# Kernel tuning notes

Measured on AMD Instinct MI355X. Metric: run time of the kernel, lower is better.

The kernel has to match this reference:

```python
import jax, jax.numpy as jnp
import numpy as np

V = 100000
E = 1600000
BN_EPS = 1e-5


def spmm(edge_index, vals, X):
    # X: (V, Cin, B); sparse L @ X via scatter-add. y[r] += w * X[c]
    rows, cols = edge_index[0], edge_index[1]
    return jnp.zeros_like(X).at[rows].add(vals[:, None, None] * X[cols])


def cheb_conv(x, edge_index, vals, w, b=None):
    # x: (B, Cin, V), w: (K, Cin, Cout) -> (B, Cout, V)
    K = w.shape[0]
    x0 = jnp.transpose(x, (2, 1, 0))  # (V, Cin, B)
    xs = [x0]
    if K > 1:
        x1 = spmm(edge_index, vals, x0)
        xs.append(x1)
        for _ in range(2, K):
            x2 = 2.0 * spmm(edge_index, vals, x1) - x0
            xs.append(x2)
            x0, x1 = x1, x2
    xk = jnp.stack(xs)  # (K, V, Cin, B)
    out = jnp.einsum('kvcb,kco->bov', xk, w)
    if b is not None:
        out = out + b[None, :, None]
    return out


def batch_norm(x, g, b):
    # training-mode BatchNorm1d on (B, C, V): stats over (B, V), biased var
    m = jnp.mean(x, axis=(0, 2), keepdims=True)
    v = jnp.var(x, axis=(0, 2), keepdims=True)
    return g[None, :, None] * (x - m) * jax.lax.rsqrt(v + BN_EPS) + b[None, :, None]


def setup_inputs() -> dict:
    key = jax.random.key(0)
    ks = jax.random.split(key, 8)
    x = jax.random.normal(ks[0], (4, 32, V), dtype=jnp.float32)
    edge_index = jax.random.randint(ks[1], (2, E), 0, V, dtype=jnp.int32)
    # small values keep the K=4 Chebyshev recursion well-scaled
    lap_vals = 0.1 * jax.random.normal(ks[2], (E,), dtype=jnp.float32)
    def w(k, K, cin, cout):
        s = 1.0 / np.sqrt(K * cin)
        return s * jax.random.normal(k, (K, cin, cout), dtype=jnp.float32)
    return {
        'x': x, 'edge_index': edge_index, 'lap_vals': lap_vals,
        'in_bn_g': jnp.ones((32,), jnp.float32), 'in_bn_b': jnp.zeros((32,), jnp.float32),
        'in_w': w(ks[3], 4, 32, 64), 'in_b': jnp.zeros((64,), jnp.float32),
        'h0_bn_g': jnp.ones((64,), jnp.float32), 'h0_bn_b': jnp.zeros((64,), jnp.float32),
        'h0_w': w(ks[4], 4, 64, 64), 'h0_b': jnp.zeros((64,), jnp.float32),
        'h1_bn_g': jnp.ones((64,), jnp.float32), 'h1_bn_b': jnp.zeros((64,), jnp.float32),
        'h1_w': w(ks[5], 4, 64, 32), 'h1_b': jnp.zeros((32,), jnp.float32),
    }


def reference(x, edge_index, lap_vals, in_bn_g, in_bn_b, in_w, in_b,
              h0_bn_g, h0_bn_b, h0_w, h0_b, h1_bn_g, h1_bn_b, h1_w, h1_b):
    xn = batch_norm(x, in_bn_g, in_bn_b)
    out = cheb_conv(xn, edge_index, lap_vals, in_w, in_b)
    # hidden layer 0
    out = jax.nn.relu(out)
    out = batch_norm(out, h0_bn_g, h0_bn_b)
    out = cheb_conv(out, edge_index, lap_vals, h0_w, h0_b)
    # hidden layer 1
    out = jax.nn.relu(out)
    out = batch_norm(out, h1_bn_g, h1_bn_b)
    out = cheb_conv(out, edge_index, lap_vals, h1_w, h1_b)
    # in_channels == out_channels -> Identity shortcut on the BN'ed input
    return jax.nn.relu(out + xn)
```

## Files before the change

kernel.cpp:

```cpp
#include <hip/hip_runtime.h>
#include <cstdint>
#include <cstddef>

#define VN 100000
#define EN 1600000
static constexpr float BN_EPS_F = 1e-5f;
static constexpr float INV_N = 1.0f / 400000.0f;

using short8 = __attribute__((ext_vector_type(8))) short;
using f32x4  = __attribute__((ext_vector_type(4))) float;

__device__ __forceinline__ float bf_lo(unsigned int p) {
  return __builtin_bit_cast(float, p << 16);
}
__device__ __forceinline__ float bf_hi(unsigned int p) {
  return __builtin_bit_cast(float, p & 0xffff0000u);
}
__device__ __forceinline__ float bf1(unsigned short u) {
  return __builtin_bit_cast(float, ((unsigned int)u) << 16);
}
__device__ __forceinline__ unsigned short f2bf(float f) {
  unsigned int x = __builtin_bit_cast(unsigned int, f);
  x += 0x7fffu + ((x >> 16) & 1u);
  return (unsigned short)(x >> 16);
}
__device__ __forceinline__ unsigned int pack2(float a, float b) {
  return (unsigned int)f2bf(a) | ((unsigned int)f2bf(b) << 16);
}

template <int EPL>
__device__ __forceinline__ void gather_accum(int start, int end,
    const int* __restrict__ cs, const float* __restrict__ vs,
    const unsigned short* __restrict__ X, int XS, int lane, float* acc) {
  int e = start;
  for (; e + 4 <= end; e += 4) {
    const int c0 = cs[e], c1 = cs[e + 1], c2 = cs[e + 2], c3 = cs[e + 3];
    const float w0 = vs[e], w1 = vs[e + 1], w2 = vs[e + 2], w3 = vs[e + 3];
    if constexpr (EPL == 4) {
      const uint2 q0 = *reinterpret_cast<const uint2*>(X + (size_t)c0 * XS + lane * 4);
      const uint2 q1 = *reinterpret_cast<const uint2*>(X + (size_t)c1 * XS + lane * 4);
      const uint2 q2 = *reinterpret_cast<const uint2*>(X + (size_t)c2 * XS + lane * 4);
      const uint2 q3 = *reinterpret_cast<const uint2*>(X + (size_t)c3 * XS + lane * 4);
      acc[0] += w0 * bf_lo(q0.x) + w1 * bf_lo(q1.x) + w2 * bf_lo(q2.x) + w3 * bf_lo(q3.x);
      acc[1] += w0 * bf_hi(q0.x) + w1 * bf_hi(q1.x) + w2 * bf_hi(q2.x) + w3 * bf_hi(q3.x);
      acc[2] += w0 * bf_lo(q0.y) + w1 * bf_lo(q1.y) + w2 * bf_lo(q2.y) + w3 * bf_lo(q3.y);
      acc[3] += w0 * bf_hi(q0.y) + w1 * bf_hi(q1.y) + w2 * bf_hi(q2.y) + w3 * bf_hi(q3.y);
    } else {
      const unsigned int q0 = *reinterpret_cast<const unsigned int*>(X + (size_t)c0 * XS + lane * 2);
      const unsigned int q1 = *reinterpret_cast<const unsigned int*>(X + (size_t)c1 * XS + lane * 2);
      const unsigned int q2 = *reinterpret_cast<const unsigned int*>(X + (size_t)c2 * XS + lane * 2);
      const unsigned int q3 = *reinterpret_cast<const unsigned int*>(X + (size_t)c3 * XS + lane * 2);
      acc[0] += w0 * bf_lo(q0) + w1 * bf_lo(q1) + w2 * bf_lo(q2) + w3 * bf_lo(q3);
      acc[1] += w0 * bf_hi(q0) + w1 * bf_hi(q1) + w2 * bf_hi(q2) + w3 * bf_hi(q3);
    }
  }
  for (; e < end; e++) {
    const int c0 = cs[e];
    const float w0 = vs[e];
    if constexpr (EPL == 4) {
      const uint2 q0 = *reinterpret_cast<const uint2*>(X + (size_t)c0 * XS + lane * 4);
      acc[0] += w0 * bf_lo(q0.x);
      acc[1] += w0 * bf_hi(q0.x);
      acc[2] += w0 * bf_lo(q0.y);
      acc[3] += w0 * bf_hi(q0.y);
    } else {
      const unsigned int q0 = *reinterpret_cast<const unsigned int*>(X + (size_t)c0 * XS + lane * 2);
      acc[0] += w0 * bf_lo(q0);
      acc[1] += w0 * bf_hi(q0);
    }
  }
}

__global__ __launch_bounds__(256) void stats_x_kernel(const float* __restrict__ x,
                                                      float* __restrict__ stats) {
  const int p = blockIdx.x & 127;
  const int chunk = blockIdx.x >> 7;
  const int c = p & 31, b = p >> 5;
  const float* base = x + ((size_t)b * 32 + c) * VN + chunk * 12500;
  float s = 0.f, s2 = 0.f;
  for (int i = threadIdx.x; i < 12500; i += 256) {
    float v = base[i];
    s += v; s2 += v * v;
  }
  __shared__ float r1[256], r2[256];
  r1[threadIdx.x] = s; r2[threadIdx.x] = s2;
  __syncthreads();
  for (int off = 128; off > 0; off >>= 1) {
    if (threadIdx.x < off) {
      r1[threadIdx.x] += r1[threadIdx.x + off];
      r2[threadIdx.x] += r2[threadIdx.x + off];
    }
    __syncthreads();
  }
  if (threadIdx.x == 0) {
    atomicAdd(&stats[c], r1[0]);
    atomicAdd(&stats[64 + c], r2[0]);
  }
}

__global__ void finalize_stats_kernel(float* __restrict__ stats,
                                      const float* __restrict__ g,
                                      const float* __restrict__ beta, int C) {
  int c = threadIdx.x;
  if (c < C) {
    float m = stats[c] * INV_N;
    float var = stats[64 + c] * INV_N - m * m;
    float sc = g[c] * rsqrtf(var + BN_EPS_F);
    stats[128 + c] = sc;
    stats[192 + c] = beta[c] - m * sc;
  }
}

__global__ __launch_bounds__(128) void bn_transpose_kernel(const float* __restrict__ x,
                                                           const float* __restrict__ stats,
                                                           unsigned short* __restrict__ xn) {
  const int tid = threadIdx.x;
  const int b = tid >> 5, c = tid & 31;
  const int v0 = blockIdx.x * 64;
  const float sc = stats[128 + c], sh = stats[192 + c];
  const float* src = x + ((size_t)b * 32 + c) * VN;
  for (int i = 0; i < 64; i++) {
    int v = v0 + i;
    if (v < VN) xn[(size_t)v * 128 + tid] = f2bf(sc * src[v] + sh);
  }
}

__global__ __launch_bounds__(256) void pack_wb_kernel(const float* __restrict__ W,
                                                      unsigned short* __restrict__ Wb,
                                                      int Cin, int Cout) {
  const int i = blockIdx.x * 256 + threadIdx.x;
  const int KC = Cin >> 5, T = Cout >> 4;
  const int tot = 4 * KC * T * 512;
  if (i >= tot) return;
  const int j = i & 7;
  const int l = (i >> 3) & 63;
  const int rem = i >> 9;
  const int t = rem % T;
  const int kc = (rem / T) % KC;
  const int k = rem / (T * KC);
  const int c = kc * 32 + (l >> 4) * 8 + j;
  const int o = t * 16 + (l & 15);
  Wb[i] = f2bf(W[((size_t)k * Cin + c) * Cout + o]);
}

__global__ __launch_bounds__(256) void hist_kernel(const int* __restrict__ rows,
                                                   int* __restrict__ cnt) {
  int i = blockIdx.x * blockDim.x + threadIdx.x;
  const int stride = gridDim.x * blockDim.x;
  for (; i < EN; i += stride) atomicAdd(&cnt[rows[i]], 1);
}

__global__ __launch_bounds__(256) void scan1_kernel(const int* __restrict__ cnt,
                                                    int* __restrict__ rp,
                                                    int* __restrict__ chunkSums) {
  __shared__ int sh[256];
  const int t = threadIdx.x;
  const int base = blockIdx.x * 2048 + t * 8;
  int vals[8]; int tot = 0;
#pragma unroll
  for (int i = 0; i < 8; i++) {
    int idx = base + i;
    int v = (idx < VN) ? cnt[idx] : 0;
    vals[i] = v; tot += v;
  }
  sh[t] = tot;
  __syncthreads();
  for (int off = 1; off < 256; off <<= 1) {
    int v = (t >= off) ? sh[t - off] : 0;
    __syncthreads();
    sh[t] += v;
    __syncthreads();
  }
  int run = sh[t] - tot;
#pragma unroll
  for (int i = 0; i < 8; i++) {
    int idx = base + i;
    if (idx < VN) rp[idx] = run;
    run += vals[i];
  }
  if (t == 255) chunkSums[blockIdx.x] = sh[255];
}

__global__ void scan2_kernel(const int* __restrict__ chunkSums,
                             int* __restrict__ chunkOff,
                             int* __restrict__ rp, int nChunks) {
  if (threadIdx.x == 0 && blockIdx.x == 0) {
    int off = 0;
    for (int j = 0; j < nChunks; j++) { chunkOff[j] = off; off += chunkSums[j]; }
    rp[VN] = off;
  }
}

__global__ __launch_bounds__(256) void scan3_kernel(int* __restrict__ rp,
                                                    const int* __restrict__ chunkOff,
                                                    int* __restrict__ fill) {
  int i = blockIdx.x * 256 + threadIdx.x;
  if (i < VN) {
    int v = rp[i] + chunkOff[i >> 11];
    rp[i] = v;
    fill[i] = v;
  }
}

__global__ __launch_bounds__(256) void fill_kernel(const int* __restrict__ rows,
                                                   const int* __restrict__ cols,
                                                   const float* __restrict__ lap,
                                                   int* __restrict__ fill,
                                                   int* __restrict__ cols_s,
                                                   float* __restrict__ vals_s) {
  int i = blockIdx.x * blockDim.x + threadIdx.x;
  const int stride = gridDim.x * blockDim.x;
  for (; i < EN; i += stride) {
    int r = rows[i];
    int pos = atomicAdd(&fill[r], 1);
    cols_s[pos] = cols[i];
    vals_s[pos] = lap[i];
  }
}

__global__ __launch_bounds__(256) void row_sum_kernel(const int* __restrict__ rp,
                                                      const float* __restrict__ vs,
                                                      float* __restrict__ rowsum) {
  const int i = blockIdx.x * 256 + threadIdx.x;
  if (i >= VN) return;
  const int s = rp[i], e = rp[i + 1];
  float acc = 0.f;
  for (int j = s; j < e; j++) acc += vs[j];
  rowsum[i] = acc;
}

template <int EPL, int MODE, bool AFFE, bool AFFP>
__global__ __launch_bounds__(256, 8) void spmm_kernel(const int* __restrict__ rp,
                                                   const int* __restrict__ cs,
                                                   const float* __restrict__ vs,
                                                   const unsigned short* __restrict__ X, int XS,
                                                   const unsigned short* __restrict__ P, int PS,
                                                   const unsigned short* __restrict__ Q, int QS,
                                                   unsigned short* __restrict__ Y, int YS,
                                                   const float* __restrict__ bnp,
                                                   const float* __restrict__ rowsum) {
  const int lane = threadIdx.x & 63;
  const int row = blockIdx.x * 4 + (threadIdx.x >> 6);
  const int start = rp[row], end = rp[row + 1];
  float acc[EPL];
#pragma unroll
  for (int j = 0; j < EPL; j++) acc[j] = 0.f;
  gather_accum<EPL>(start, end, cs, vs, X, XS, lane, acc);

  if constexpr (EPL == 4) {
    float4 sc, sh;
    if constexpr (AFFE || AFFP) {
      const int c0 = (lane * 4) & 63;
      sc = *reinterpret_cast<const float4*>(bnp + c0);
      sh = *reinterpret_cast<const float4*>(bnp + 64 + c0);
    }
    float r0 = acc[0], r1 = acc[1], r2 = acc[2], r3 = acc[3];
    if constexpr (AFFE) {
      const float rs = rowsum[row];
      r0 = sc.x * r0 + rs * sh.x;
      r1 = sc.y * r1 + rs * sh.y;
      r2 = sc.z * r2 + rs * sh.z;
      r3 = sc.w * r3 + rs * sh.w;
    }
    if constexpr (MODE == 1) {
      const uint2 p = *reinterpret_cast<const uint2*>(P + (size_t)row * PS + lane * 4);
      float p0 = bf_lo(p.x), p1 = bf_hi(p.x), p2 = bf_lo(p.y), p3 = bf_hi(p.y);
      if constexpr (AFFP) {
        p0 = p0 * sc.x + sh.x;
        p1 = p1 * sc.y + sh.y;
        p2 = p2 * sc.z + sh.z;
        p3 = p3 * sc.w + sh.w;
      }
      r0 = 2.f * r0 - p0;
      r1 = 2.f * r1 - p1;
      r2 = 2.f * r2 - p2;
      r3 = 2.f * r3 - p3;
    }
    uint2 r;
    r.x = pack2(r0, r1);
    r.y = pack2(r2, r3);
    *reinterpret_cast<uint2*>(Y + (size_t)row * YS + lane * 4) = r;
  } else {
    float r0 = acc[0], r1 = acc[1];
    if constexpr (MODE == 1) {
      const unsigned int p = *reinterpret_cast<const unsigned int*>(P + (size_t)row * PS + lane * 2);
      r0 = 2.f * r0 - bf_lo(p);
      r1 = 2.f * r1 - bf_hi(p);
    } else if constexpr (MODE == 2) {
      const unsigned int p = *reinterpret_cast<const unsigned int*>(P + (size_t)row * PS + lane * 2);
      r0 = 2.f * r0 + bf_lo(p);
      r1 = 2.f * r1 + bf_hi(p);
    } else if constexpr (MODE == 3) {
      const unsigned int p = *reinterpret_cast<const unsigned int*>(P + (size_t)row * PS + lane * 2);
      const unsigned int qq = *reinterpret_cast<const unsigned int*>(Q + (size_t)row * QS + lane * 2);
      r0 = 2.f * r0 - bf_lo(qq) + bf_lo(p);
      r1 = 2.f * r1 - bf_hi(qq) + bf_hi(p);
    } else if constexpr (MODE == 4) {
      const unsigned int p = *reinterpret_cast<const unsigned int*>(P + (size_t)row * PS + lane * 2);
      const unsigned int qq = *reinterpret_cast<const unsigned int*>(Q + (size_t)row * QS + lane * 2);
      r0 = r0 - bf_lo(qq) + bf_lo(p);
      r1 = r1 - bf_hi(qq) + bf_hi(p);
    }
    *reinterpret_cast<unsigned int*>(Y + (size_t)row * YS + lane * 2) = pack2(r0, r1);
  }
}

template <int Cin, int Cout, int X0S, int X1S, int X2S, bool AFF0>
__global__ __launch_bounds__(256, 8) void fused_cheb_kernel(const int* __restrict__ rp,
                                                         const int* __restrict__ cs,
                                                         const float* __restrict__ vs,
                                                         const unsigned short* __restrict__ X0,
                                                         const unsigned short* __restrict__ X1,
                                                         const unsigned short* __restrict__ X2,
                                                         unsigned short* __restrict__ OUT,
                                                         const unsigned short* __restrict__ Wb,
                                                         const float* __restrict__ Bias,
                                                         const float* __restrict__ bnp) {
  constexpr int EPL = Cin * 4 / 64;
  constexpr int ROWSH = Cin * 4;
  __shared__ unsigned short t3s[4 * ROWSH];
  const int lane = threadIdx.x & 63;
  const int wv = threadIdx.x >> 6;
  const int row0 = blockIdx.x * 4;
  const int row = row0 + wv;

  float g[EPL];
#pragma unroll
  for (int j = 0; j < EPL; j++) g[j] = 0.f;
  const int start = rp[row], end = rp[row + 1];
  gather_accum<EPL>(start, end, cs, vs, X2, X2S, lane, g);
  {
    unsigned int* tw = reinterpret_cast<unsigned int*>(t3s + wv * ROWSH);
    if constexpr (EPL == 4) {
      const uint2 p = *reinterpret_cast<const uint2*>(X1 + (size_t)row * X1S + lane * 4);
      tw[lane * 2]     = pack2(2.f * g[0] - bf_lo(p.x), 2.f * g[1] - bf_hi(p.x));
      tw[lane * 2 + 1] = pack2(2.f * g[2] - bf_lo(p.y), 2.f * g[3] - bf_hi(p.y));
    } else {
      const unsigned int p = *reinterpret_cast<const unsigned int*>(X1 + (size_t)row * X1S + lane * 2);
      tw[lane] = pack2(2.f * g[0] - bf_lo(p), 2.f * g[1] - bf_hi(p));
    }
  }
  __syncthreads();

  constexpr int KC = Cin / 32;
  constexpr int T = Cout / 16;
  const int col = lane & 15, quad = lane >> 4;
  const int t = wv % T;
  const int ar = col >> 2, ab = col & 3;

  const unsigned short* xa0 = X0 + (size_t)(row0 + ar) * X0S + ab * Cin + quad * 8;
  const unsigned short* xa1 = X1 + (size_t)(row0 + ar) * X1S + ab * Cin + quad * 8;
  const unsigned short* xa2 = X2 + (size_t)(row0 + ar) * X2S + ab * Cin + quad * 8;
  const unsigned short* wb = Wb + (size_t)t * 512 + lane * 8;

  f32x4 acc = {0.f, 0.f, 0.f, 0.f};
#pragma unroll
  for (int kc = 0; kc < KC; kc++) {
    short8 af;
    if constexpr (AFF0) {
      const short8 raw = *reinterpret_cast<const short8*>(xa0 + kc * 32);
      const int cb = quad * 8 + kc * 32;
      const float4 s0 = *reinterpret_cast<const float4*>(bnp + cb);
      const float4 s1 = *reinterpret_cast<const float4*>(bnp + cb + 4);
      const float4 t0 = *reinterpret_cast<const float4*>(bnp + 64 + cb);
      const float4 t1 = *reinterpret_cast<const float4*>(bnp + 64 + cb + 4);
      const float scv[8] = {s0.x, s0.y, s0.z, s0.w, s1.x, s1.y, s1.z, s1.w};
      const float shv[8] = {t0.x, t0.y, t0.z, t0.w, t1.x, t1.y, t1.z, t1.w};
#pragma unroll
      for (int j = 0; j < 8; j++) {
        float v = bf1((unsigned short)raw[j]) * scv[j] + shv[j];
        af[j] = (short)f2bf(v);
      }
    } else {
      af = *reinterpret_cast<const short8*>(xa0 + kc * 32);
    }
    const short8 bf = *reinterpret_cast<const short8*>(wb + (size_t)(0 * KC + kc) * T * 512);
    acc = __builtin_amdgcn_mfma_f32_16x16x32_bf16(af, bf, acc, 0, 0, 0);
  }
#pragma unroll
  for (int kc = 0; kc < KC; kc++) {
    const short8 af = *reinterpret_cast<const short8*>(xa1 + kc * 32);
    const short8 bf = *reinterpret_cast<const short8*>(wb + (size_t)(1 * KC + kc) * T * 512);
    acc = __builtin_amdgcn_mfma_f32_16x16x32_bf16(af, bf, acc, 0, 0, 0);
  }
#pragma unroll
  for (int kc = 0; kc < KC; kc++) {
    const short8 af = *reinterpret_cast<const short8*>(xa2 + kc * 32);
    const short8 bf = *reinterpret_cast<const short8*>(wb + (size_t)(2 * KC + kc) * T * 512);
    acc = __builtin_amdgcn_mfma_f32_16x16x32_bf16(af, bf, acc, 0, 0, 0);
  }
#pragma unroll
  for (int kc = 0; kc < KC; kc++) {
    const short8 af = *reinterpret_cast<const short8*>(&t3s[ar * ROWSH + ab * Cin + kc * 32 + quad * 8]);
    const short8 bf = *reinterpret_cast<const short8*>(wb + (size_t)(3 * KC + kc) * T * 512);
    acc = __builtin_amdgcn_mfma_f32_16x16x32_bf16(af, bf, acc, 0, 0, 0);
  }
  __syncthreads();

  if (T == 4 || wv < 2) {
    const int og = t * 16 + col;
    const float bs = Bias[og];
#pragma unroll
    for (int r = 0; r < 4; r++) {
      const float val = fmaxf(acc[r] + bs, 0.f);
      OUT[(size_t)(row0 + quad) * 256 + r * Cout + og] = f2bf(val);
    }
  }
}

__global__ __launch_bounds__(256, 8) void gemm_z_kernel(const unsigned short* __restrict__ A,
                                                        const unsigned short* __restrict__ Wb,
                                                        const float* __restrict__ Bias,
                                                        unsigned short* __restrict__ zA,
                                                        unsigned short* __restrict__ zB,
                                                        const float* __restrict__ bnp) {
  const int lane = threadIdx.x & 63;
  const int wv = threadIdx.x >> 6;
  const int row0 = blockIdx.x * 4;
  const int col = lane & 15, quad = lane >> 4;
  const int ar = col >> 2, ab = col & 3;
  const unsigned short* xa = A + (size_t)(row0 + ar) * 256 + ab * 64 + quad * 8;
  const unsigned short* wb = Wb + (size_t)wv * 4 * 512 + lane * 8;
  unsigned short* zr = (wv < 2) ? (zA + (size_t)wv * VN * 128)
                                : (zB + (size_t)(wv - 2) * VN * 128);
  short8 afr[2];
#pragma unroll
  for (int kc = 0; kc < 2; kc++) {
    const short8 raw = *reinterpret_cast<const short8*>(xa + kc * 32);
    const int cb = quad * 8 + kc * 32;
    const float4 s0 = *reinterpret_cast<const float4*>(bnp + cb);
    const float4 s1 = *reinterpret_cast<const float4*>(bnp + cb + 4);
    const float4 t0 = *reinterpret_cast<const float4*>(bnp + 64 + cb);
    const float4 t1 = *reinterpret_cast<const float4*>(bnp + 64 + cb + 4);
    const float scv[8] = {s0.x, s0.y, s0.z, s0.w, s1.x, s1.y, s1.z, s1.w};
    const float shv[8] = {t0.x, t0.y, t0.z, t0.w, t1.x, t1.y, t1.z, t1.w};
#pragma unroll
    for (int j = 0; j < 8; j++) {
      float v = bf1((unsigned short)raw[j]) * scv[j] + shv[j];
      afr[kc][j] = (short)f2bf(v);
    }
  }
#pragma unroll
  for (int t = 0; t < 2; t++) {
    f32x4 acc = {0.f, 0.f, 0.f, 0.f};
#pragma unroll
    for (int kc = 0; kc < 2; kc++) {
      const short8 bf = *reinterpret_cast<const short8*>(wb + (size_t)(kc * 2 + t) * 512);
      acc = __builtin_amdgcn_mfma_f32_16x16x32_bf16(afr[kc], bf, acc, 0, 0, 0);
    }
    const int og = t * 16 + col;
    const float bs = (wv == 0) ? Bias[og] : 0.f;
#pragma unroll
    for (int r = 0; r < 4; r++) {
      zr[(size_t)(row0 + quad) * 128 + r * 32 + og] = f2bf(acc[r] + bs);
    }
  }
}

__global__ __launch_bounds__(256) void stats_out_kernel(const unsigned short* __restrict__ SRC,
                                                        float* __restrict__ stats) {
  const int tid = threadIdx.x;
  const int per = (VN + gridDim.x - 1) / gridDim.x;
  const int v0 = blockIdx.x * per;
  const int v1 = (v0 + per < VN) ? (v0 + per) : VN;
  float s = 0.f, s2 = 0.f;
  for (int v = v0; v < v1; v++) {
    float val = bf1(SRC[(size_t)v * 256 + tid]);
    s += val; s2 += val * val;
  }
  __shared__ float r1[256], r2[256];
  r1[tid] = s; r2[tid] = s2;
  __syncthreads();
  if (tid < 64) {
    float a = r1[tid] + r1[tid + 64] + r1[tid + 128] + r1[tid + 192];
    float b = r2[tid] + r2[tid + 64] + r2[tid + 128] + r2[tid + 192];
    atomicAdd(&stats[tid], a);
    atomicAdd(&stats[64 + tid], b);
  }
}

__global__ __launch_bounds__(256) void final_kernel(const unsigned short* __restrict__ SRC,
                                                    const unsigned short* __restrict__ xn,
                                                    float* __restrict__ out) {
  const int lane = threadIdx.x & 63;
  const int grp = threadIdx.x >> 6;
  const int v = blockIdx.x * 64 + lane;
  if (v >= VN) return;
  for (int ob = grp; ob < 128; ob += 4) {
    float val = bf1(SRC[(size_t)v * 128 + ob]) + bf1(xn[(size_t)v * 128 + ob]);
    val = fmaxf(val, 0.f);
    out[(size_t)ob * VN + v] = val;
  }
}

static constexpr size_t align_up(size_t x) { return (x + 255) & ~(size_t)255; }
static constexpr size_t OFF_RP    = 0;
static constexpr size_t OFF_FILL  = align_up(OFF_RP + (size_t)(VN + 1) * 4);
static constexpr size_t OFF_CHS   = align_up(OFF_FILL + (size_t)VN * 4);
static constexpr size_t OFF_CHO   = align_up(OFF_CHS + 256);
static constexpr size_t OFF_STATS = align_up(OFF_CHO + 256);
static constexpr size_t OFF_WP    = align_up(OFF_STATS + 1024);
static constexpr size_t OFF_CS    = align_up(OFF_WP + 32768 * 2);
static constexpr size_t OFF_VS    = align_up(OFF_CS + (size_t)EN * 4);
static constexpr size_t OFF_XN    = align_up(OFF_VS + (size_t)EN * 4);
static constexpr size_t OFF_XL    = align_up(OFF_XN + (size_t)VN * 128 * 2);
static constexpr size_t OFF_A     = align_up(OFF_XL + (size_t)VN * 256 * 2);
static constexpr size_t OFF_B     = align_up(OFF_A + (size_t)VN * 256 * 2);
static constexpr size_t OFF_END   = OFF_B + (size_t)VN * 256 * 2;

extern "C" void kernel_launch(void* const* d_in, const int* in_sizes, int n_in,
                              void* d_out, int out_size, void* d_ws, size_t ws_size,
                              hipStream_t stream) {
  if (ws_size < OFF_END) return;

  const float* x       = (const float*)d_in[0];
  const int*   rows    = (const int*)d_in[1];
  const int*   cols    = rows + EN;
  const float* lap     = (const float*)d_in[2];
  const float* in_bn_g = (const float*)d_in[3];
  const float* in_bn_b = (const float*)d_in[4];
  const float* in_w    = (const float*)d_in[5];
  const float* in_b    = (const float*)d_in[6];
  const float* h0_bn_g = (const float*)d_in[7];
  const float* h0_bn_b = (const float*)d_in[8];
  const float* h0_w    = (const float*)d_in[9];
  const float* h0_b    = (const float*)d_in[10];
  const float* h1_bn_g = (const float*)d_in[11];
  const float* h1_bn_b = (const float*)d_in[12];
  const float* h1_w    = (const float*)d_in[13];
  const float* h1_b    = (const float*)d_in[14];
  float* outp = (float*)d_out;

  char* ws = (char*)d_ws;
  int*   rp     = (int*)(ws + OFF_RP);
  int*   fill   = (int*)(ws + OFF_FILL);
  float* rowsum = (float*)(ws + OFF_FILL);
  int*   chS    = (int*)(ws + OFF_CHS);
  int*   chO    = (int*)(ws + OFF_CHO);
  float* stats  = (float*)(ws + OFF_STATS);
  unsigned short* wbIn = (unsigned short*)(ws + OFF_WP);
  unsigned short* wbH0 = wbIn + 8192;
  unsigned short* wbH1 = wbH0 + 16384;
  int*   cs     = (int*)(ws + OFF_CS);
  float* vs     = (float*)(ws + OFF_VS);
  unsigned short* xn = (unsigned short*)(ws + OFF_XN);
  unsigned short* XL = (unsigned short*)(ws + OFF_XL);
  unsigned short* A  = (unsigned short*)(ws + OFF_A);
  unsigned short* B  = (unsigned short*)(ws + OFF_B);
  const float* bnp = stats + 128;

  const int nChunks = (VN + 2047) / 2048;

  pack_wb_kernel<<<32, 256, 0, stream>>>(in_w, wbIn, 32, 64);
  pack_wb_kernel<<<64, 256, 0, stream>>>(h0_w, wbH0, 64, 64);
  pack_wb_kernel<<<32, 256, 0, stream>>>(h1_w, wbH1, 64, 32);

  hipMemsetAsync(stats, 0, 1024, stream);
  stats_x_kernel<<<1024, 256, 0, stream>>>(x, stats);
  finalize_stats_kernel<<<1, 64, 0, stream>>>(stats, in_bn_g, in_bn_b, 32);
  bn_transpose_kernel<<<1563, 128, 0, stream>>>(x, stats, xn);

  hipMemsetAsync(fill, 0, (size_t)VN * 4, stream);
  hist_kernel<<<2048, 256, 0, stream>>>(rows, fill);
  scan1_kernel<<<nChunks, 256, 0, stream>>>(fill, rp, chS);
  scan2_kernel<<<1, 64, 0, stream>>>(chS, chO, rp, nChunks);
  scan3_kernel<<<(VN + 255) / 256, 256, 0, stream>>>(rp, chO, fill);
  fill_kernel<<<2048, 256, 0, stream>>>(rows, cols, lap, fill, cs, vs);
  row_sum_kernel<<<(VN + 255) / 256, 256, 0, stream>>>(rp, vs, rowsum);

  unsigned short* XLa = XL;
  unsigned short* XLb = XL + (size_t)VN * 128;
  spmm_kernel<2, 0, false, false><<<VN / 4, 256, 0, stream>>>(
      rp, cs, vs, xn, 128, nullptr, 0, nullptr, 0, XLa, 128, nullptr, nullptr);
  spmm_kernel<2, 1, false, false><<<VN / 4, 256, 0, stream>>>(
      rp, cs, vs, XLa, 128, xn, 128, nullptr, 0, XLb, 128, nullptr, nullptr);
  fused_cheb_kernel<32, 64, 128, 128, 128, false><<<VN / 4, 256, 0, stream>>>(
      rp, cs, vs, xn, XLa, XLb, A, wbIn, in_b, nullptr);
  hipMemsetAsync(stats, 0, 1024, stream);
  stats_out_kernel<<<256, 256, 0, stream>>>(A, stats);
  finalize_stats_kernel<<<1, 64, 0, stream>>>(stats, h0_bn_g, h0_bn_b, 64);

  spmm_kernel<4, 0, true, false><<<VN / 4, 256, 0, stream>>>(
      rp, cs, vs, A, 256, nullptr, 0, nullptr, 0, XL, 256, bnp, rowsum);
  spmm_kernel<4, 1, false, true><<<VN / 4, 256, 0, stream>>>(
      rp, cs, vs, XL, 256, A, 256, nullptr, 0, B, 256, bnp, nullptr);
  fused_cheb_kernel<64, 64, 256, 256, 256, true><<<VN / 4, 256, 0, stream>>>(
      rp, cs, vs, A, XL, B, A, wbH0, h0_b, bnp);
  hipMemsetAsync(stats, 0, 1024, stream);
  stats_out_kernel<<<256, 256, 0, stream>>>(A, stats);
  finalize_stats_kernel<<<1, 64, 0, stream>>>(stats, h1_bn_g, h1_bn_b, 64);

  {
    unsigned short* z0 = XL;
    unsigned short* z1 = XL + (size_t)VN * 128;
    unsigned short* z2 = B;
    unsigned short* z3 = B + (size_t)VN * 128;
    gemm_z_kernel<<<VN / 4, 256, 0, stream>>>(A, wbH1, h1_b, z0, z2, bnp);
    spmm_kernel<2, 2, false, false><<<VN / 4, 256, 0, stream>>>(
        rp, cs, vs, z3, 128, z2, 128, nullptr, 0, z2, 128, nullptr, nullptr);
    spmm_kernel<2, 3, false, false><<<VN / 4, 256, 0, stream>>>(
        rp, cs, vs, z2, 128, z1, 128, z3, 128, z1, 128, nullptr, nullptr);
    spmm_kernel<2, 4, false, false><<<VN / 4, 256, 0, stream>>>(
        rp, cs, vs, z1, 128, z0, 128, z2, 128, z0, 128, nullptr, nullptr);
    final_kernel<<<1563, 256, 0, stream>>>(z0, xn, outp);
  }
}
```

Before: 1.665 ms.

## Fold batch-norm affine into packed weights and biases; unroll gather by eight

Moves the per-element batch-norm scale and shift out of the fused Chebyshev and gemm_z kernels. The scale is folded into the packed bf16 weights, and the shift times the weights is folded into per-k bias vectors computed by a small new kernel. Weight packing for the hidden layers now runs after their stats are finalized. Separately, the sparse gather loop is unrolled to eight edges so more loads are in flight. The change drops per-element conversion work but alters bf16 rounding order and adds two tiny serial launches per layer.

```diff
diff --git a/kernel.cpp b/kernel.cpp
--- a/kernel.cpp
+++ b/kernel.cpp
@@ -33,40 +33,77 @@
     const int* __restrict__ cs, const float* __restrict__ vs,
     const unsigned short* __restrict__ X, int XS, int lane, float* acc) {
   int e = start;
-  for (; e + 4 <= end; e += 4) {
-    const int c0 = cs[e], c1 = cs[e + 1], c2 = cs[e + 2], c3 = cs[e + 3];
-    const float w0 = vs[e], w1 = vs[e + 1], w2 = vs[e + 2], w3 = vs[e + 3];
-    if constexpr (EPL == 4) {
-      const uint2 q0 = *reinterpret_cast<const uint2*>(X + (size_t)c0 * XS + lane * 4);
-      const uint2 q1 = *reinterpret_cast<const uint2*>(X + (size_t)c1 * XS + lane * 4);
-      const uint2 q2 = *reinterpret_cast<const uint2*>(X + (size_t)c2 * XS + lane * 4);
-      const uint2 q3 = *reinterpret_cast<const uint2*>(X + (size_t)c3 * XS + lane * 4);
-      acc[0] += w0 * bf_lo(q0.x) + w1 * bf_lo(q1.x) + w2 * bf_lo(q2.x) + w3 * bf_lo(q3.x);
-      acc[1] += w0 * bf_hi(q0.x) + w1 * bf_hi(q1.x) + w2 * bf_hi(q2.x) + w3 * bf_hi(q3.x);
-      acc[2] += w0 * bf_lo(q0.y) + w1 * bf_lo(q1.y) + w2 * bf_lo(q2.y) + w3 * bf_lo(q3.y);
-      acc[3] += w0 * bf_hi(q0.y) + w1 * bf_hi(q1.y) + w2 * bf_hi(q2.y) + w3 * bf_hi(q3.y);
-    } else {
-      const unsigned int q0 = *reinterpret_cast<const unsigned int*>(X + (size_t)c0 * XS + lane * 2);
-      const unsigned int q1 = *reinterpret_cast<const unsigned int*>(X + (size_t)c1 * XS + lane * 2);
-      const unsigned int q2 = *reinterpret_cast<const unsigned int*>(X + (size_t)c2 * XS + lane * 2);
-      const unsigned int q3 = *reinterpret_cast<const unsigned int*>(X + (size_t)c3 * XS + lane * 2);
-      acc[0] += w0 * bf_lo(q0) + w1 * bf_lo(q1) + w2 * bf_lo(q2) + w3 * bf_lo(q3);
-      acc[1] += w0 * bf_hi(q0) + w1 * bf_hi(q1) + w2 * bf_hi(q2) + w3 * bf_hi(q3);
-    }
-  }
-  for (; e < end; e++) {
-    const int c0 = cs[e];
-    const float w0 = vs[e];
-    if constexpr (EPL == 4) {
-      const uint2 q0 = *reinterpret_cast<const uint2*>(X + (size_t)c0 * XS + lane * 4);
-      acc[0] += w0 * bf_lo(q0.x);
-      acc[1] += w0 * bf_hi(q0.x);
-      acc[2] += w0 * bf_lo(q0.y);
-      acc[3] += w0 * bf_hi(q0.y);
-    } else {
-      const unsigned int q0 = *reinterpret_cast<const unsigned int*>(X + (size_t)c0 * XS + lane * 2);
-      acc[0] += w0 * bf_lo(q0);
-      acc[1] += w0 * bf_hi(q0);
+  if constexpr (EPL == 4) {
+    for (; e + 8 <= end; e += 8) {
+      uint2 q[8]; float w[8];
+#pragma unroll
+      for (int u = 0; u < 8; u++) {
+        q[u] = *reinterpret_cast<const uint2*>(X + (size_t)cs[e + u] * XS + lane * 4);
+        w[u] = vs[e + u];
+      }
+#pragma unroll
+      for (int u = 0; u < 8; u++) {
+        acc[0] += w[u] * bf_lo(q[u].x);
+        acc[1] += w[u] * bf_hi(q[u].x);
+        acc[2] += w[u] * bf_lo(q[u].y);
+        acc[3] += w[u] * bf_hi(q[u].y);
+      }
+    }
+    for (; e + 4 <= end; e += 4) {
+      uint2 q[4]; float w[4];
+#pragma unroll
+      for (int u = 0; u < 4; u++) {
+        q[u] = *reinterpret_cast<const uint2*>(X + (size_t)cs[e + u] * XS + lane * 4);
+        w[u] = vs[e + u];
+      }
+#pragma unroll
+      for (int u = 0; u < 4; u++) {
+        acc[0] += w[u] * bf_lo(q[u].x);
+        acc[1] += w[u] * bf_hi(q[u].x);
+        acc[2] += w[u] * bf_lo(q[u].y);
+        acc[3] += w[u] * bf_hi(q[u].y);
+      }
+    }
+    for (; e < end; e++) {
+      const uint2 q = *reinterpret_cast<const uint2*>(X + (size_t)cs[e] * XS + lane * 4);
+      const float w = vs[e];
+      acc[0] += w * bf_lo(q.x);
+      acc[1] += w * bf_hi(q.x);
+      acc[2] += w * bf_lo(q.y);
+      acc[3] += w * bf_hi(q.y);
+    }
+  } else {
+    for (; e + 8 <= end; e += 8) {
+      unsigned int q[8]; float w[8];
+#pragma unroll
+      for (int u = 0; u < 8; u++) {
+        q[u] = *reinterpret_cast<const unsigned int*>(X + (size_t)cs[e + u] * XS + lane * 2);
+        w[u] = vs[e + u];
+      }
+#pragma unroll
+      for (int u = 0; u < 8; u++) {
+        acc[0] += w[u] * bf_lo(q[u]);
+        acc[1] += w[u] * bf_hi(q[u]);
+      }
+    }
+    for (; e + 4 <= end; e += 4) {
+      unsigned int q[4]; float w[4];
+#pragma unroll
+      for (int u = 0; u < 4; u++) {
+        q[u] = *reinterpret_cast<const unsigned int*>(X + (size_t)cs[e + u] * XS + lane * 2);
+        w[u] = vs[e + u];
+      }
+#pragma unroll
+      for (int u = 0; u < 4; u++) {
+        acc[0] += w[u] * bf_lo(q[u]);
+        acc[1] += w[u] * bf_hi(q[u]);
+      }
+    }
+    for (; e < end; e++) {
+      const unsigned int q = *reinterpret_cast<const unsigned int*>(X + (size_t)cs[e] * XS + lane * 2);
+      const float w = vs[e];
+      acc[0] += w * bf_lo(q);
+      acc[1] += w * bf_hi(q);
     }
   }
 }
@@ -127,7 +164,9 @@
 
 __global__ __launch_bounds__(256) void pack_wb_kernel(const float* __restrict__ W,
                                                       unsigned short* __restrict__ Wb,
-                                                      int Cin, int Cout) {
+                                                      int Cin, int Cout,
+                                                      const float* __restrict__ scale,
+                                                      int kmask) {
   const int i = blockIdx.x * 256 + threadIdx.x;
   const int KC = Cin >> 5, T = Cout >> 4;
   const int tot = 4 * KC * T * 512;
@@ -140,7 +179,23 @@
   const int k = rem / (T * KC);
   const int c = kc * 32 + (l >> 4) * 8 + j;
   const int o = t * 16 + (l & 15);
-  Wb[i] = f2bf(W[((size_t)k * Cin + c) * Cout + o]);
+  float w = W[((size_t)k * Cin + c) * Cout + o];
+  if (scale != nullptr && ((kmask >> k) & 1)) w *= scale[c];
+  Wb[i] = f2bf(w);
+}
+
+__global__ void bias_fold_kernel(const float* __restrict__ W,
+                                 const float* __restrict__ b0,
+                                 const float* __restrict__ stats,
+                                 float* __restrict__ out,
+                                 int Cin, int Cout, int K) {
+  const int i = threadIdx.x;
+  if (i >= K * Cout) return;
+  const int k = i / Cout, o = i % Cout;
+  const float* sh = stats + 192;
+  float acc = (k == 0) ? b0[o] : 0.f;
+  for (int c = 0; c < Cin; c++) acc += sh[c] * W[((size_t)k * Cin + c) * Cout + o];
+  out[i] = acc;
 }
 
 __global__ __launch_bounds__(256) void hist_kernel(const int* __restrict__ rows,
@@ -305,7 +360,7 @@
   }
 }
 
-template <int Cin, int Cout, int X0S, int X1S, int X2S, bool AFF0>
+template <int Cin, int Cout, int X0S, int X1S, int X2S>
 __global__ __launch_bounds__(256, 8) void fused_cheb_kernel(const int* __restrict__ rp,
                                                          const int* __restrict__ cs,
                                                          const float* __restrict__ vs,
@@ -314,8 +369,7 @@
                                                          const unsigned short* __restrict__ X2,
                                                          unsigned short* __restrict__ OUT,
                                                          const unsigned short* __restrict__ Wb,
-                                                         const float* __restrict__ Bias,
-                                                         const float* __restrict__ bnp) {
+                                                         const float* __restrict__ Bias) {
   constexpr int EPL = Cin * 4 / 64;
   constexpr int ROWSH = Cin * 4;
   __shared__ unsigned short t3s[4 * ROWSH];
@@ -356,24 +410,7 @@
   f32x4 acc = {0.f, 0.f, 0.f, 0.f};
 #pragma unroll
   for (int kc = 0; kc < KC; kc++) {
-    short8 af;
-    if constexpr (AFF0) {
-      const short8 raw = *reinterpret_cast<const short8*>(xa0 + kc * 32);
-      const int cb = quad * 8 + kc * 32;
-      const float4 s0 = *reinterpret_cast<const float4*>(bnp + cb);
-      const float4 s1 = *reinterpret_cast<const float4*>(bnp + cb + 4);
-      const float4 t0 = *reinterpret_cast<const float4*>(bnp + 64 + cb);
-      const float4 t1 = *reinterpret_cast<const float4*>(bnp + 64 + cb + 4);
-      const float scv[8] = {s0.x, s0.y, s0.z, s0.w, s1.x, s1.y, s1.z, s1.w};
-      const float shv[8] = {t0.x, t0.y, t0.z, t0.w, t1.x, t1.y, t1.z, t1.w};
-#pragma unroll
-      for (int j = 0; j < 8; j++) {
-        float v = bf1((unsigned short)raw[j]) * scv[j] + shv[j];
-        af[j] = (short)f2bf(v);
-      }
-    } else {
-      af = *reinterpret_cast<const short8*>(xa0 + kc * 32);
-    }
+    const short8 af = *reinterpret_cast<const short8*>(xa0 + kc * 32);
     const short8 bf = *reinterpret_cast<const short8*>(wb + (size_t)(0 * KC + kc) * T * 512);
     acc = __builtin_amdgcn_mfma_f32_16x16x32_bf16(af, bf, acc, 0, 0, 0);
   }
@@ -410,10 +447,9 @@
 
 __global__ __launch_bounds__(256, 8) void gemm_z_kernel(const unsigned short* __restrict__ A,
                                                         const unsigned short* __restrict__ Wb,
-                                                        const float* __restrict__ Bias,
+                                                        const float* __restrict__ zb,
                                                         unsigned short* __restrict__ zA,
-                                                        unsigned short* __restrict__ zB,
-                                                        const float* __restrict__ bnp) {
+                                                        unsigned short* __restrict__ zB) {
   const int lane = threadIdx.x & 63;
   const int wv = threadIdx.x >> 6;
   const int row0 = blockIdx.x * 4;
@@ -423,33 +459,17 @@
   const unsigned short* wb = Wb + (size_t)wv * 4 * 512 + lane * 8;
   unsigned short* zr = (wv < 2) ? (zA + (size_t)wv * VN * 128)
                                 : (zB + (size_t)(wv - 2) * VN * 128);
-  short8 afr[2];
-#pragma unroll
-  for (int kc = 0; kc < 2; kc++) {
-    const short8 raw = *reinterpret_cast<const short8*>(xa + kc * 32);
-    const int cb = quad * 8 + kc * 32;
-    const float4 s0 = *reinterpret_cast<const float4*>(bnp + cb);
-    const float4 s1 = *reinterpret_cast<const float4*>(bnp + cb + 4);
-    const float4 t0 = *reinterpret_cast<const float4*>(bnp + 64 + cb);
-    const float4 t1 = *reinterpret_cast<const float4*>(bnp + 64 + cb + 4);
-    const float scv[8] = {s0.x, s0.y, s0.z, s0.w, s1.x, s1.y, s1.z, s1.w};
-    const float shv[8] = {t0.x, t0.y, t0.z, t0.w, t1.x, t1.y, t1.z, t1.w};
-#pragma unroll
-    for (int j = 0; j < 8; j++) {
-      float v = bf1((unsigned short)raw[j]) * scv[j] + shv[j];
-      afr[kc][j] = (short)f2bf(v);
-    }
-  }
+  const short8 af0 = *reinterpret_cast<const short8*>(xa);
+  const short8 af1 = *reinterpret_cast<const short8*>(xa + 32);
 #pragma unroll
   for (int t = 0; t < 2; t++) {
     f32x4 acc = {0.f, 0.f, 0.f, 0.f};
-#pragma unroll
-    for (int kc = 0; kc < 2; kc++) {
-      const short8 bf = *reinterpret_cast<const short8*>(wb + (size_t)(kc * 2 + t) * 512);
-      acc = __builtin_amdgcn_mfma_f32_16x16x32_bf16(afr[kc], bf, acc, 0, 0, 0);
-    }
+    const short8 bf0 = *reinterpret_cast<const short8*>(wb + (size_t)(0 * 2 + t) * 512);
+    const short8 bf1 = *reinterpret_cast<const short8*>(wb + (size_t)(1 * 2 + t) * 512);
+    acc = __builtin_amdgcn_mfma_f32_16x16x32_bf16(af0, bf0, acc, 0, 0, 0);
+    acc = __builtin_amdgcn_mfma_f32_16x16x32_bf16(af1, bf1, acc, 0, 0, 0);
     const int og = t * 16 + col;
-    const float bs = (wv == 0) ? Bias[og] : 0.f;
+    const float bs = zb[wv * 32 + og];
 #pragma unroll
     for (int r = 0; r < 4; r++) {
       zr[(size_t)(row0 + quad) * 128 + r * 32 + og] = f2bf(acc[r] + bs);
@@ -499,7 +519,8 @@
 static constexpr size_t OFF_CHS   = align_up(OFF_FILL + (size_t)VN * 4);
 static constexpr size_t OFF_CHO   = align_up(OFF_CHS + 256);
 static constexpr size_t OFF_STATS = align_up(OFF_CHO + 256);
-static constexpr size_t OFF_WP    = align_up(OFF_STATS + 1024);
+static constexpr size_t OFF_BIAS  = align_up(OFF_STATS + 1024);
+static constexpr size_t OFF_WP    = align_up(OFF_BIAS + 1024);
 static constexpr size_t OFF_CS    = align_up(OFF_WP + 32768 * 2);
 static constexpr size_t OFF_VS    = align_up(OFF_CS + (size_t)EN * 4);
 static constexpr size_t OFF_XN    = align_up(OFF_VS + (size_t)EN * 4);
@@ -538,6 +559,7 @@
   int*   chS    = (int*)(ws + OFF_CHS);
   int*   chO    = (int*)(ws + OFF_CHO);
   float* stats  = (float*)(ws + OFF_STATS);
+  float* biasF  = (float*)(ws + OFF_BIAS);
   unsigned short* wbIn = (unsigned short*)(ws + OFF_WP);
   unsigned short* wbH0 = wbIn + 8192;
   unsigned short* wbH1 = wbH0 + 16384;
@@ -551,9 +573,7 @@
 
   const int nChunks = (VN + 2047) / 2048;
 
-  pack_wb_kernel<<<32, 256, 0, stream>>>(in_w, wbIn, 32, 64);
-  pack_wb_kernel<<<64, 256, 0, stream>>>(h0_w, wbH0, 64, 64);
-  pack_wb_kernel<<<32, 256, 0, stream>>>(h1_w, wbH1, 64, 32);
+  pack_wb_kernel<<<32, 256, 0, stream>>>(in_w, wbIn, 32, 64, nullptr, 0);
 
   hipMemsetAsync(stats, 0, 1024, stream);
   stats_x_kernel<<<1024, 256, 0, stream>>>(x, stats);
@@ -574,28 +594,34 @@
       rp, cs, vs, xn, 128, nullptr, 0, nullptr, 0, XLa, 128, nullptr, nullptr);
   spmm_kernel<2, 1, false, false><<<VN / 4, 256, 0, stream>>>(
       rp, cs, vs, XLa, 128, xn, 128, nullptr, 0, XLb, 128, nullptr, nullptr);
-  fused_cheb_kernel<32, 64, 128, 128, 128, false><<<VN / 4, 256, 0, stream>>>(
-      rp, cs, vs, xn, XLa, XLb, A, wbIn, in_b, nullptr);
+  fused_cheb_kernel<32, 64, 128, 128, 128><<<VN / 4, 256, 0, stream>>>(
+      rp, cs, vs, xn, XLa, XLb, A, wbIn, in_b);
   hipMemsetAsync(stats, 0, 1024, stream);
   stats_out_kernel<<<256, 256, 0, stream>>>(A, stats);
   finalize_stats_kernel<<<1, 64, 0, stream>>>(stats, h0_bn_g, h0_bn_b, 64);
+
+  pack_wb_kernel<<<64, 256, 0, stream>>>(h0_w, wbH0, 64, 64, bnp, 0x1);
+  bias_fold_kernel<<<1, 128, 0, stream>>>(h0_w, h0_b, stats, biasF, 64, 64, 1);
 
   spmm_kernel<4, 0, true, false><<<VN / 4, 256, 0, stream>>>(
       rp, cs, vs, A, 256, nullptr, 0, nullptr, 0, XL, 256, bnp, rowsum);
   spmm_kernel<4, 1, false, true><<<VN / 4, 256, 0, stream>>>(
       rp, cs, vs, XL, 256, A, 256, nullptr, 0, B, 256, bnp, nullptr);
-  fused_cheb_kernel<64, 64, 256, 256, 256, true><<<VN / 4, 256, 0, stream>>>(
-      rp, cs, vs, A, XL, B, A, wbH0, h0_b, bnp);
+  fused_cheb_kernel<64, 64, 256, 256, 256><<<VN / 4, 256, 0, stream>>>(
+      rp, cs, vs, A, XL, B, A, wbH0, biasF);
   hipMemsetAsync(stats, 0, 1024, stream);
   stats_out_kernel<<<256, 256, 0, stream>>>(A, stats);
   finalize_stats_kernel<<<1, 64, 0, stream>>>(stats, h1_bn_g, h1_bn_b, 64);
+
+  pack_wb_kernel<<<32, 256, 0, stream>>>(h1_w, wbH1, 64, 32, bnp, 0xF);
+  bias_fold_kernel<<<1, 128, 0, stream>>>(h1_w, h1_b, stats, biasF + 64, 64, 32, 4);
 
   {
     unsigned short* z0 = XL;
     unsigned short* z1 = XL + (size_t)VN * 128;
     unsigned short* z2 = B;
     unsigned short* z3 = B + (size_t)VN * 128;
-    gemm_z_kernel<<<VN / 4, 256, 0, stream>>>(A, wbH1, h1_b, z0, z2, bnp);
+    gemm_z_kernel<<<VN / 4, 256, 0, stream>>>(A, wbH1, biasF + 64, z0, z2);
     spmm_kernel<2, 2, false, false><<<VN / 4, 256, 0, stream>>>(
         rp, cs, vs, z3, 128, z2, 128, nullptr, 0, z2, 128, nullptr, nullptr);
     spmm_kernel<2, 3, false, false><<<VN / 4, 256, 0, stream>>>(
```

After: 1.604 ms. 3.7% less time.
